# Kernel optimization log

Measured on AMD Instinct MI355X. Metric: run time of the kernel, lower is better.

Reference implementation:

```python
import jax, jax.numpy as jnp
import numpy as np

B, A, HR = 2, 180, 512
H_OUT = W_OUT = 512


def setup_inputs() -> dict:
    key = jax.random.key(0)
    k1, = jax.random.split(key, 1)
    sino = jax.random.normal(k1, (B, A, HR), dtype=jnp.float32)
    angles_deg = jnp.linspace(0.0, 180.0, A, endpoint=False, dtype=jnp.float32)
    return {"sino": sino, "angles_deg": angles_deg, "H": H_OUT, "W": W_OUT}


def _forward(sino, angles_deg, H, W):
    Bn, An, Hr = sino.shape
    pad = int(1.0 * 0.1 * min(H, W))  # pad_ratio = 1.0
    Hp, Wp = H + 2 * pad, W + 2 * pad

    # --- F.interpolate bilinear, align_corners=False: (A,B,Hr,1) -> (A,B,Hp,Wp).
    # Input width is 1, so width interp replicates the single column; only height interp matters.
    src = jnp.clip((jnp.arange(Hp, dtype=jnp.float32) + 0.5) * (Hr / Hp) - 0.5, 0.0, Hr - 1)
    i0 = jnp.floor(src).astype(jnp.int32)
    i1 = jnp.minimum(i0 + 1, Hr - 1)
    wH = src - i0.astype(jnp.float32)
    p = jnp.transpose(sino, (1, 0, 2)).astype(jnp.float32)  # (A,B,Hr)
    col = p[:, :, i0] * (1.0 - wH) + p[:, :, i1] * wH       # (A,B,Hp)
    proj = jnp.broadcast_to(col[:, :, :, None], (An, Bn, Hp, Wp))  # (A,B,Hp,Wp)

    # --- affine_grid (align_corners=False), sign = -1
    th = -jnp.deg2rad(angles_deg)
    c, s = jnp.cos(th), jnp.sin(th)                          # (A,)
    xs = (jnp.arange(Wp, dtype=jnp.float32) + 0.5) * (2.0 / Wp) - 1.0
    ys = (jnp.arange(Hp, dtype=jnp.float32) + 0.5) * (2.0 / Hp) - 1.0
    gx = c[:, None, None] * xs[None, None, :] - s[:, None, None] * ys[None, :, None]  # (A,Hp,Wp)
    gy = s[:, None, None] * xs[None, None, :] + c[:, None, None] * ys[None, :, None]

    # --- grid_sample bilinear, zeros padding, align_corners=False
    ix = ((gx + 1.0) * Wp - 1.0) * 0.5
    iy = ((gy + 1.0) * Hp - 1.0) * 0.5
    x0 = jnp.floor(ix).astype(jnp.int32); x1 = x0 + 1
    y0 = jnp.floor(iy).astype(jnp.int32); y1 = y0 + 1
    wx = ix - x0.astype(jnp.float32)
    wy = iy - y0.astype(jnp.float32)

    def corner(img, xi, yi, w):  # img (B,Hp,Wp); idx/w (Hp,Wp)
        valid = (xi >= 0) & (xi <= Wp - 1) & (yi >= 0) & (yi <= Hp - 1)
        xc = jnp.clip(xi, 0, Wp - 1)
        yc = jnp.clip(yi, 0, Hp - 1)
        return img[:, yc, xc] * (w * valid.astype(jnp.float32))[None]

    def sample(img, x0a, x1a, y0a, y1a, wxa, wya):
        return (corner(img, x0a, y0a, (1 - wxa) * (1 - wya)) +
                corner(img, x1a, y0a, wxa * (1 - wya)) +
                corner(img, x0a, y1a, (1 - wxa) * wya) +
                corner(img, x1a, y1a, wxa * wya))

    xr = jax.vmap(sample)(proj, x0, x1, y0, y1, wx, wy)      # (A,B,Hp,Wp)
    acc = xr.sum(axis=0) / (An + 1e-06)                      # (B,Hp,Wp)
    acc = acc[:, None, :, :]                                 # (B,1,Hp,Wp)
    if pad > 0:
        acc = acc[:, :, pad:Hp - pad, pad:Wp - pad]
    return acc


def reference(sino, angles_deg, H, W):
    return _forward(sino, angles_deg, H, W)
```

## Files before the change

### kernel.cpp

```cpp
#include <hip/hip_runtime.h>
#include <hip/hip_fp16.h>
#include <math.h>

#define B_N   2
#define A_N   180
#define HR_N  512
#define H_OUT 512
#define W_OUT 512
#define PAD   51
#define HP    614
#define WP    614
#define GUARD 80
#define HPP   (HP + 2*GUARD)
#define NPIX  (H_OUT * W_OUT)

#define TW    16
#define TH    8
#define QA    45
#define CH_Q  15
#define NCH   3
#define WIN   20


__device__ __forceinline__ float col_val(const float* __restrict__ sino,
                                         int b, int a, int yy) {
    if (yy < 0 || yy >= HP) return 0.0f;
    float src = ((float)yy + 0.5f) * ((float)HR_N / (float)HP) - 0.5f;
    src = fminf(fmaxf(src, 0.0f), (float)(HR_N - 1));
    int i0 = (int)floorf(src);
    int i1 = min(i0 + 1, HR_N - 1);
    float wH = src - (float)i0;
    const float* srow = sino + ((size_t)b * A_N + a) * HR_N;
    return srow[i0] * (1.0f - wH) + srow[i1] * wH;
}

__global__ void prep_kernel(const float* __restrict__ sino,
                            const float* __restrict__ angles,
                            uint2* __restrict__ pk2,
                            float2* __restrict__ tg) {
    int idx = blockIdx.x * blockDim.x + threadIdx.x;
    if (idx < A_N) {
        float th = -angles[idx] * (float)(M_PI / 180.0);
        tg[idx] = make_float2(cosf(th), sinf(th));
    }
    const int total = A_N * HPP;
    if (idx < total) {
        int y = idx % HPP;
        int a = idx / HPP;
        int yy = y - GUARD;
        float v00 = col_val(sino, 0, a, yy);
        float v10 = col_val(sino, 1, a, yy);
        float v01 = col_val(sino, 0, a, yy + 1);
        float v11 = col_val(sino, 1, a, yy + 1);
        __half2 lo = __floats2half2_rn(v00, v10);
        __half2 hi = __floats2half2_rn(v01, v11);
        uint2 u;
        u.x = *(unsigned int*)&lo;
        u.y = *(unsigned int*)&hi;
        pk2[idx] = u;
    }
}

template <bool INTERIOR>
__device__ __forceinline__ void bp_body(const uint2* __restrict__ pk2,
                                        const float2* __restrict__ s_tg,
                                        const int* __restrict__ s_base,
                                        uint2* __restrict__ s_win,
                                        int t, int q, float X, float Y,
                                        float Xc, float Yc,
                                        float& a00, float& a01, float& a10, float& a11) {
    for (int ch = 0; ch < NCH; ++ch) {
        for (int e = t; e < 4 * CH_Q * WIN; e += 256) {
            int wid = e / WIN;
            int j   = e - wid * WIN;
            int qq  = wid / CH_Q;
            int la  = wid - qq * CH_Q;
            int a   = qq * QA + ch * CH_Q + la;
            s_win[e] = pk2[(size_t)a * HPP + (GUARD + s_base[a] + j)];
        }
        __syncthreads();

        const int abase = q * QA + ch * CH_Q;
        const int wbase = q * (CH_Q * WIN);
        if (INTERIOR) {
            __half2 h0 = __float2half2_rn(0.0f);
            __half2 h1 = __float2half2_rn(0.0f);
#pragma unroll
            for (int la = 0; la < CH_Q; ++la) {
                float2 cs = s_tg[abase + la];
                float c = cs.x, s = cs.y;
                float iyc = fmaf(s, Xc, fmaf(c, Yc, 306.5f));
                float Kf  = 315.5f - floorf(iyc);
                float f0  = fmaf(s, X, fmaf(c, Y, Kf));
                float f1  = f0 + s;
                int   li0 = (int)f0;  float wy0 = f0 - (float)li0;
                int   li1 = (int)f1;  float wy1 = f1 - (float)li1;
                uint2 cv0 = s_win[wbase + la * WIN + li0];
                uint2 cv1 = s_win[wbase + la * WIN + li1];
                __half2 lo0 = *(__half2*)&cv0.x, hi0 = *(__half2*)&cv0.y;
                __half2 lo1 = *(__half2*)&cv1.x, hi1 = *(__half2*)&cv1.y;
                h0 = __hadd2(h0, __hfma2(__float2half2_rn(wy0), __hsub2(hi0, lo0), lo0));
                h1 = __hadd2(h1, __hfma2(__float2half2_rn(wy1), __hsub2(hi1, lo1), lo1));
            }
            a00 += __low2float(h0);  a01 += __high2float(h0);
            a10 += __low2float(h1);  a11 += __high2float(h1);
        } else {
#pragma unroll
            for (int la = 0; la < CH_Q; ++la) {
                float2 cs = s_tg[abase + la];
                float c = cs.x, s = cs.y;
                float iyc = fmaf(s, Xc, fmaf(c, Yc, 306.5f));
                float Kf  = 315.5f - floorf(iyc);
                float f0  = fmaf(s, X, fmaf(c, Y, Kf));
                float f1  = f0 + s;
                int   li0 = (int)f0;  float wy0 = f0 - (float)li0;
                int   li1 = (int)f1;  float wy1 = f1 - (float)li1;
                uint2 cv0 = s_win[wbase + la * WIN + li0];
                uint2 cv1 = s_win[wbase + la * WIN + li1];
                __half2 lo0 = *(__half2*)&cv0.x, hi0 = *(__half2*)&cv0.y;
                __half2 lo1 = *(__half2*)&cv1.x, hi1 = *(__half2*)&cv1.y;
                __half2 r0 = __hfma2(__float2half2_rn(wy0), __hsub2(hi0, lo0), lo0);
                __half2 r1 = __hfma2(__float2half2_rn(wy1), __hsub2(hi1, lo1), lo1);
                float ix0 = fmaf(c, X, fmaf(-s, Y, 306.5f));
                float ix1 = ix0 + c;
                float xf0 = fminf(fmaxf(ix0 + 1.0f, 0.0f), 1.0f)
                          * fminf(fmaxf((float)WP - ix0, 0.0f), 1.0f);
                float xf1 = fminf(fmaxf(ix1 + 1.0f, 0.0f), 1.0f)
                          * fminf(fmaxf((float)WP - ix1, 0.0f), 1.0f);
                a00 = fmaf(xf0, __low2float(r0),  a00);
                a01 = fmaf(xf0, __high2float(r0), a01);
                a10 = fmaf(xf1, __low2float(r1),  a10);
                a11 = fmaf(xf1, __high2float(r1), a11);
            }
        }
        __syncthreads();
    }
}

__global__ __launch_bounds__(256, 8) void bp_kernel(const uint2* __restrict__ pk2,
                                                    const float2* __restrict__ tgv,
                                                    float* __restrict__ out) {
    __shared__ float2 s_tg[A_N];
    __shared__ int    s_base[A_N];
    __shared__ uint2  s_win[4 * CH_Q * WIN];
    __shared__ float  s_red[3][256];

    int t  = threadIdx.x;
    int tx = blockIdx.x, ty = blockIdx.y;
    float Xc = (float)(tx * TW) - 248.0f;
    float Yc = (float)(ty * TH) - 252.0f;

    if (t < A_N) {
        float2 cs = tgv[t];
        s_tg[t] = cs;
        float iyc = fmaf(cs.y, Xc, fmaf(cs.x, Yc, 306.5f));
        s_base[t] = (int)floorf(iyc) - 9;
    }

    int q  = t >> 6;
    int tt = t & 63;
    int lx = (tt & 7) << 1;
    int ly = tt >> 3;
    float X = (float)(tx * TW + lx) - 255.5f;
    float Y = (float)(ty * TH + ly) - 255.5f;

    float a00 = 0.0f, a01 = 0.0f, a10 = 0.0f, a11 = 0.0f;
    __syncthreads();

    bool interior = (Xc * Xc + Yc * Yc) <= 87500.0f;
    if (interior)
        bp_body<true >(pk2, s_tg, s_base, s_win, t, q, X, Y, Xc, Yc, a00, a01, a10, a11);
    else
        bp_body<false>(pk2, s_tg, s_base, s_win, t, q, X, Y, Xc, Yc, a00, a01, a10, a11);

    int pix = ly * TW + lx;
    if (q != 0) {
        s_red[q - 1][pix]           = a00;
        s_red[q - 1][pix + 1]       = a10;
        s_red[q - 1][128 + pix]     = a01;
        s_red[q - 1][128 + pix + 1] = a11;
    }
    __syncthreads();
    if (q == 0) {
        const float inv = 1.0f / (180.0f + 1e-6f);
        float r00 = (a00 + s_red[0][pix]       + s_red[1][pix]       + s_red[2][pix])       * inv;
        float r10 = (a10 + s_red[0][pix+1]     + s_red[1][pix+1]     + s_red[2][pix+1])     * inv;
        float r01 = (a01 + s_red[0][128+pix]   + s_red[1][128+pix]   + s_red[2][128+pix])   * inv;
        float r11 = (a11 + s_red[0][128+pix+1] + s_red[1][128+pix+1] + s_red[2][128+pix+1]) * inv;
        int idx = (ty * TH + ly) * W_OUT + (tx * TW + lx);
        out[idx]            = r00;
        out[idx + 1]        = r10;
        out[NPIX + idx]     = r01;
        out[NPIX + idx + 1] = r11;
    }
}

extern "C" void kernel_launch(void* const* d_in, const int* in_sizes, int n_in,
                              void* d_out, int out_size, void* d_ws, size_t ws_size,
                              hipStream_t stream) {
    const float* sino   = (const float*)d_in[0];
    const float* angles = (const float*)d_in[1];
    char*   ws  = (char*)d_ws;
    uint2*  pk2 = (uint2*)ws;
    float2* tg  = (float2*)(ws + (size_t)A_N * HPP * sizeof(uint2));

    const int total = A_N * HPP;
    prep_kernel<<<(total + 255) / 256, 256, 0, stream>>>(sino, angles, pk2, tg);

    dim3 grid(W_OUT / TW, H_OUT / TH);
    bp_kernel<<<grid, 256, 0, stream>>>(pk2, tg, (float*)d_out);
}
```

Measured before the change: 83.40 us.

## Double-buffer sinogram window loads with register prefetch across angle chunks

```diff
diff --git a/kernel.cpp b/kernel.cpp
--- a/kernel.cpp
+++ b/kernel.cpp
@@ -20,6 +20,9 @@
 #define CH_Q  15
 #define NCH   3
 #define WIN   20
+#define NE    (4 * CH_Q * WIN)
+#define K_IT  5
+#define TAIL  (NE - 256 * (K_IT - 1))
 
 
 __device__ __forceinline__ float col_val(const float* __restrict__ sino,
@@ -61,89 +64,118 @@
     }
 }
 
+
+__device__ __forceinline__ void pf_load(uint2* pf, const int* code,
+                                        const unsigned* s_off,
+                                        const uint2* __restrict__ pk2,
+                                        int ch, int t) {
+#pragma unroll
+    for (int k = 0; k < K_IT; ++k) {
+        if (k < K_IT - 1 || t < TAIL) {
+            int a = (code[k] >> 5) + ch * CH_Q;
+            pf[k] = pk2[s_off[a] + (unsigned)(code[k] & 31)];
+        }
+    }
+}
+
+__device__ __forceinline__ void pf_store(const uint2* pf, uint2* buf, int t) {
+#pragma unroll
+    for (int k = 0; k < K_IT; ++k) {
+        if (k < K_IT - 1 || t < TAIL)
+            buf[t + 256 * k] = pf[k];
+    }
+}
+
+
 template <bool INTERIOR>
-__device__ __forceinline__ void bp_body(const uint2* __restrict__ pk2,
-                                        const float2* __restrict__ s_tg,
-                                        const int* __restrict__ s_base,
-                                        uint2* __restrict__ s_win,
-                                        int t, int q, float X, float Y,
-                                        float Xc, float Yc,
-                                        float& a00, float& a01, float& a10, float& a11) {
-    for (int ch = 0; ch < NCH; ++ch) {
-        for (int e = t; e < 4 * CH_Q * WIN; e += 256) {
-            int wid = e / WIN;
-            int j   = e - wid * WIN;
-            int qq  = wid / CH_Q;
-            int la  = wid - qq * CH_Q;
-            int a   = qq * QA + ch * CH_Q + la;
-            s_win[e] = pk2[(size_t)a * HPP + (GUARD + s_base[a] + j)];
+__device__ __forceinline__ void compute_chunk(const uint2* __restrict__ w,
+                                              const float4* __restrict__ s_cs,
+                                              int abase, float X, float Y,
+                                              float& a00, float& a01, float& a10, float& a11) {
+    if (INTERIOR) {
+        __half2 h0 = __float2half2_rn(0.0f);
+        __half2 h1 = __float2half2_rn(0.0f);
+#pragma unroll
+        for (int la = 0; la < CH_Q; ++la) {
+            float4 cs = s_cs[abase + la];
+            float c = cs.x, s = cs.y;
+            float f0 = fmaf(s, X, fmaf(c, Y, cs.z));
+            float f1 = f0 + s;
+            int   li0 = (int)f0;  float wy0 = __builtin_amdgcn_fractf(f0);
+            int   li1 = (int)f1;  float wy1 = f1 - (float)li1;
+            uint2 cv0 = w[la * WIN + li0];
+            uint2 cv1 = w[la * WIN + li1];
+            __half2 lo0 = *(__half2*)&cv0.x, hi0 = *(__half2*)&cv0.y;
+            __half2 lo1 = *(__half2*)&cv1.x, hi1 = *(__half2*)&cv1.y;
+            h0 = __hadd2(h0, __hfma2(__float2half2_rn(wy0), __hsub2(hi0, lo0), lo0));
+            h1 = __hadd2(h1, __hfma2(__float2half2_rn(wy1), __hsub2(hi1, lo1), lo1));
         }
-        __syncthreads();
-
-        const int abase = q * QA + ch * CH_Q;
-        const int wbase = q * (CH_Q * WIN);
-        if (INTERIOR) {
-            __half2 h0 = __float2half2_rn(0.0f);
-            __half2 h1 = __float2half2_rn(0.0f);
-#pragma unroll
-            for (int la = 0; la < CH_Q; ++la) {
-                float2 cs = s_tg[abase + la];
-                float c = cs.x, s = cs.y;
-                float iyc = fmaf(s, Xc, fmaf(c, Yc, 306.5f));
-                float Kf  = 315.5f - floorf(iyc);
-                float f0  = fmaf(s, X, fmaf(c, Y, Kf));
-                float f1  = f0 + s;
-                int   li0 = (int)f0;  float wy0 = f0 - (float)li0;
-                int   li1 = (int)f1;  float wy1 = f1 - (float)li1;
-                uint2 cv0 = s_win[wbase + la * WIN + li0];
-                uint2 cv1 = s_win[wbase + la * WIN + li1];
-                __half2 lo0 = *(__half2*)&cv0.x, hi0 = *(__half2*)&cv0.y;
-                __half2 lo1 = *(__half2*)&cv1.x, hi1 = *(__half2*)&cv1.y;
-                h0 = __hadd2(h0, __hfma2(__float2half2_rn(wy0), __hsub2(hi0, lo0), lo0));
-                h1 = __hadd2(h1, __hfma2(__float2half2_rn(wy1), __hsub2(hi1, lo1), lo1));
-            }
-            a00 += __low2float(h0);  a01 += __high2float(h0);
-            a10 += __low2float(h1);  a11 += __high2float(h1);
-        } else {
-#pragma unroll
-            for (int la = 0; la < CH_Q; ++la) {
-                float2 cs = s_tg[abase + la];
-                float c = cs.x, s = cs.y;
-                float iyc = fmaf(s, Xc, fmaf(c, Yc, 306.5f));
-                float Kf  = 315.5f - floorf(iyc);
-                float f0  = fmaf(s, X, fmaf(c, Y, Kf));
-                float f1  = f0 + s;
-                int   li0 = (int)f0;  float wy0 = f0 - (float)li0;
-                int   li1 = (int)f1;  float wy1 = f1 - (float)li1;
-                uint2 cv0 = s_win[wbase + la * WIN + li0];
-                uint2 cv1 = s_win[wbase + la * WIN + li1];
-                __half2 lo0 = *(__half2*)&cv0.x, hi0 = *(__half2*)&cv0.y;
-                __half2 lo1 = *(__half2*)&cv1.x, hi1 = *(__half2*)&cv1.y;
-                __half2 r0 = __hfma2(__float2half2_rn(wy0), __hsub2(hi0, lo0), lo0);
-                __half2 r1 = __hfma2(__float2half2_rn(wy1), __hsub2(hi1, lo1), lo1);
-                float ix0 = fmaf(c, X, fmaf(-s, Y, 306.5f));
-                float ix1 = ix0 + c;
-                float xf0 = fminf(fmaxf(ix0 + 1.0f, 0.0f), 1.0f)
-                          * fminf(fmaxf((float)WP - ix0, 0.0f), 1.0f);
-                float xf1 = fminf(fmaxf(ix1 + 1.0f, 0.0f), 1.0f)
-                          * fminf(fmaxf((float)WP - ix1, 0.0f), 1.0f);
-                a00 = fmaf(xf0, __low2float(r0),  a00);
-                a01 = fmaf(xf0, __high2float(r0), a01);
-                a10 = fmaf(xf1, __low2float(r1),  a10);
-                a11 = fmaf(xf1, __high2float(r1), a11);
-            }
+        a00 += __low2float(h0);  a01 += __high2float(h0);
+        a10 += __low2float(h1);  a11 += __high2float(h1);
+    } else {
+#pragma unroll
+        for (int la = 0; la < CH_Q; ++la) {
+            float4 cs = s_cs[abase + la];
+            float c = cs.x, s = cs.y;
+            float f0 = fmaf(s, X, fmaf(c, Y, cs.z));
+            float f1 = f0 + s;
+            int   li0 = (int)f0;  float wy0 = __builtin_amdgcn_fractf(f0);
+            int   li1 = (int)f1;  float wy1 = f1 - (float)li1;
+            uint2 cv0 = w[la * WIN + li0];
+            uint2 cv1 = w[la * WIN + li1];
+            __half2 lo0 = *(__half2*)&cv0.x, hi0 = *(__half2*)&cv0.y;
+            __half2 lo1 = *(__half2*)&cv1.x, hi1 = *(__half2*)&cv1.y;
+            __half2 r0 = __hfma2(__float2half2_rn(wy0), __hsub2(hi0, lo0), lo0);
+            __half2 r1 = __hfma2(__float2half2_rn(wy1), __hsub2(hi1, lo1), lo1);
+            float ix0 = fmaf(c, X, fmaf(-s, Y, 306.5f));
+            float ix1 = ix0 + c;
+            float xf0 = fminf(fmaxf(ix0 + 1.0f, 0.0f), 1.0f)
+                      * fminf(fmaxf((float)WP - ix0, 0.0f), 1.0f);
+            float xf1 = fminf(fmaxf(ix1 + 1.0f, 0.0f), 1.0f)
+                      * fminf(fmaxf((float)WP - ix1, 0.0f), 1.0f);
+            a00 = fmaf(xf0, __low2float(r0),  a00);
+            a01 = fmaf(xf0, __high2float(r0), a01);
+            a10 = fmaf(xf1, __low2float(r1),  a10);
+            a11 = fmaf(xf1, __high2float(r1), a11);
         }
-        __syncthreads();
-    }
-}
-
-__global__ __launch_bounds__(256, 8) void bp_kernel(const uint2* __restrict__ pk2,
+    }
+}
+
+
+template <bool INTERIOR>
+__device__ __forceinline__ void pipeline(const uint2* __restrict__ pk2,
+                                         const float4* s_cs, const unsigned* s_off,
+                                         uint2* s_win, const int* code, int t, int q,
+                                         float X, float Y,
+                                         float& a00, float& a01, float& a10, float& a11) {
+    uint2 pf[K_IT];
+    const uint2* wq0 = s_win + q * (CH_Q * WIN);
+    const uint2* wq1 = wq0 + NE;
+    const int ab = q * QA;
+
+    pf_load(pf, code, s_off, pk2, 0, t);
+    pf_store(pf, s_win, t);
+    __syncthreads();
+
+    pf_load(pf, code, s_off, pk2, 1, t);
+    compute_chunk<INTERIOR>(wq0, s_cs, ab, X, Y, a00, a01, a10, a11);
+    pf_store(pf, s_win + NE, t);
+    __syncthreads();
+
+    pf_load(pf, code, s_off, pk2, 2, t);
+    compute_chunk<INTERIOR>(wq1, s_cs, ab + CH_Q, X, Y, a00, a01, a10, a11);
+    pf_store(pf, s_win, t);
+    __syncthreads();
+
+    compute_chunk<INTERIOR>(wq0, s_cs, ab + 2 * CH_Q, X, Y, a00, a01, a10, a11);
+}
+
+__global__ __launch_bounds__(256, 6) void bp_kernel(const uint2* __restrict__ pk2,
                                                     const float2* __restrict__ tgv,
                                                     float* __restrict__ out) {
-    __shared__ float2 s_tg[A_N];
-    __shared__ int    s_base[A_N];
-    __shared__ uint2  s_win[4 * CH_Q * WIN];
-    __shared__ float  s_red[3][256];
+    __shared__ float4   s_cs[A_N];
+    __shared__ unsigned s_off[A_N];
+    __shared__ uint2    s_win[2 * NE];
 
     int t  = threadIdx.x;
     int tx = blockIdx.x, ty = blockIdx.y;
@@ -152,9 +184,21 @@
 
     if (t < A_N) {
         float2 cs = tgv[t];
-        s_tg[t] = cs;
         float iyc = fmaf(cs.y, Xc, fmaf(cs.x, Yc, 306.5f));
-        s_base[t] = (int)floorf(iyc) - 9;
+        int base = (int)floorf(iyc) - 9;
+        s_cs[t]  = make_float4(cs.x, cs.y, 306.5f - (float)base, 0.0f);
+        s_off[t] = (unsigned)(t * HPP + GUARD + base);
+    }
+
+    int code[K_IT];
+#pragma unroll
+    for (int k = 0; k < K_IT; ++k) {
+        int e   = t + 256 * k;
+        int wid = e / WIN;
+        int j   = e - wid * WIN;
+        int qq  = wid / CH_Q;
+        int la  = wid - qq * CH_Q;
+        code[k] = ((qq * QA + la) << 5) | j;
     }
 
     int q  = t >> 6;
@@ -169,24 +213,25 @@
 
     bool interior = (Xc * Xc + Yc * Yc) <= 87500.0f;
     if (interior)
-        bp_body<true >(pk2, s_tg, s_base, s_win, t, q, X, Y, Xc, Yc, a00, a01, a10, a11);
+        pipeline<true >(pk2, s_cs, s_off, s_win, code, t, q, X, Y, a00, a01, a10, a11);
     else
-        bp_body<false>(pk2, s_tg, s_base, s_win, t, q, X, Y, Xc, Yc, a00, a01, a10, a11);
-
+        pipeline<false>(pk2, s_cs, s_off, s_win, code, t, q, X, Y, a00, a01, a10, a11);
+
+    float* s_red = (float*)(s_win + NE);
     int pix = ly * TW + lx;
     if (q != 0) {
-        s_red[q - 1][pix]           = a00;
-        s_red[q - 1][pix + 1]       = a10;
-        s_red[q - 1][128 + pix]     = a01;
-        s_red[q - 1][128 + pix + 1] = a11;
+        s_red[(q - 1) * 256 + pix]             = a00;
+        s_red[(q - 1) * 256 + pix + 1]         = a10;
+        s_red[(q - 1) * 256 + 128 + pix]       = a01;
+        s_red[(q - 1) * 256 + 128 + pix + 1]   = a11;
     }
     __syncthreads();
     if (q == 0) {
         const float inv = 1.0f / (180.0f + 1e-6f);
-        float r00 = (a00 + s_red[0][pix]       + s_red[1][pix]       + s_red[2][pix])       * inv;
-        float r10 = (a10 + s_red[0][pix+1]     + s_red[1][pix+1]     + s_red[2][pix+1])     * inv;
-        float r01 = (a01 + s_red[0][128+pix]   + s_red[1][128+pix]   + s_red[2][128+pix])   * inv;
-        float r11 = (a11 + s_red[0][128+pix+1] + s_red[1][128+pix+1] + s_red[2][128+pix+1]) * inv;
+        float r00 = (a00 + s_red[pix]           + s_red[256 + pix]           + s_red[512 + pix])           * inv;
+        float r10 = (a10 + s_red[pix + 1]       + s_red[256 + pix + 1]       + s_red[512 + pix + 1])       * inv;
+        float r01 = (a01 + s_red[128 + pix]     + s_red[256 + 128 + pix]     + s_red[512 + 128 + pix])     * inv;
+        float r11 = (a11 + s_red[128 + pix + 1] + s_red[256 + 128 + pix + 1] + s_red[512 + 128 + pix + 1]) * inv;
         int idx = (ty * TH + ly) * W_OUT + (tx * TW + lx);
         out[idx]            = r00;
         out[idx + 1]        = r10;
```

New measurement: 266.1 us. 3.19x slower.
